# Optimization experiments

Hardware: AMD Instinct MI355X
Metric: run time of the kernel (lower is better)

## Reference

```python
import jax, jax.numpy as jnp
import numpy as np

B, S, D, H = 512, 256, 2, 256


def _lstm_cell(x, h, c, W_ih, W_hh, b_ih, b_hh):
    # PyTorch gate order: i, f, g, o
    gates = x @ W_ih.T + b_ih + h @ W_hh.T + b_hh
    i, f, g, o = jnp.split(gates, 4, axis=-1)
    c_new = jax.nn.sigmoid(f) * c + jax.nn.sigmoid(i) * jnp.tanh(g)
    h_new = jax.nn.sigmoid(o) * jnp.tanh(c_new)
    return h_new, c_new


def setup_inputs() -> dict:
    key = jax.random.key(0)
    ks = jax.random.split(key, 9)
    bound = 1.0 / np.sqrt(H)
    u = lambda k, shp: jax.random.uniform(k, shp, jnp.float32, -bound, bound)
    return {
        "inputs": jax.random.normal(ks[0], (B, S, D), jnp.float32),
        "enc_W_ih": u(ks[1], (4 * H, D)),
        "enc_W_hh": u(ks[2], (4 * H, H)),
        "enc_b_ih": u(ks[3], (4 * H,)),
        "enc_b_hh": u(ks[4], (4 * H,)),
        "dec_W_ih": u(ks[5], (4 * H, H)),
        "dec_W_hh": u(ks[6], (4 * H, H)),
        "dec_b_ih": u(ks[7], (4 * H,)),
        "dec_b_hh": u(ks[8], (4 * H,)),
    }


def reference(inputs, enc_W_ih, enc_W_hh, enc_b_ih, enc_b_hh,
              dec_W_ih, dec_W_hh, dec_b_ih, dec_b_hh):
    bsz, seq_len, _ = inputs.shape
    hid = enc_W_hh.shape[1]

    # ---- encoder LSTM (batch_first), h0 = c0 = 0 ----
    h0 = jnp.zeros((bsz, hid), inputs.dtype)
    c0 = jnp.zeros((bsz, hid), inputs.dtype)

    def enc_step(carry, x_t):
        h, c = carry
        h, c = _lstm_cell(x_t, h, c, enc_W_ih, enc_W_hh, enc_b_ih, enc_b_hh)
        return (h, c), h

    (h_last, c_last), enc_out_t = jax.lax.scan(enc_step, (h0, c0), inputs.transpose(1, 0, 2))
    enc_out = enc_out_t.transpose(1, 0, 2)  # [B, S, H]

    key = jax.random.key(42)
    keys = jax.random.split(key, seq_len)
    dec_in0 = jnp.zeros((bsz, hid), inputs.dtype)
    mask0 = jnp.zeros((bsz, seq_len), dtype=bool)
    rows = jnp.arange(bsz)

    def dec_step(carry, k):
        dec_in, h, c, mask = carry
        h, c = _lstm_cell(dec_in, h, c, dec_W_ih, dec_W_hh, dec_b_ih, dec_b_hh)
        scores = jnp.einsum('bsh,bh->bs', enc_out, h)          # bmm attention
        scores = jnp.where(mask, -jnp.inf, scores)             # mask visited
        idx = jax.random.categorical(k, scores, axis=1)        # multinomial(softmax)
        mask = mask.at[rows, idx].set(True)
        dec_in = jnp.take_along_axis(enc_out, idx[:, None, None], axis=1)[:, 0, :]
        return (dec_in, h, c, mask), idx

    _, indices_t = jax.lax.scan(dec_step, (dec_in0, h_last, c_last, mask0), keys)
    return indices_t.T  # [B, S] int
```

## Files before the change

### kernel.cpp

```cpp
#include <hip/hip_runtime.h>
#include <cstdint>
#include <cstddef>


typedef float v4f __attribute__((ext_vector_type(4)));
typedef float v2f __attribute__((ext_vector_type(2)));
typedef unsigned long long u64;

#define WS_HX_OFF     0x000000u
#define WS_GX_OFF     0x100000u
#define WS_AMX_OFF    0x200000u
#define WS_GFLAG_OFF  0x204000u
#define WS_SYNC_BYTES 0x205000u
#define WS_ENCW2_OFF  0x300000u
#define WS_DECWI4_OFF 0x400000u
#define WS_DECWH4_OFF 0x500000u
#define WS_ENCK4_OFF  0x600000u
#define WS_NEEDED     ((size_t)WS_ENCK4_OFF + (size_t)512 * 64 * 256 * 16)

__device__ __forceinline__ unsigned rotl32(unsigned x, int r) {
  return (x << r) | (x >> (32 - r));
}
__device__ __forceinline__ float sigm(float x) { return 1.f / (1.f + expf(-x)); }

__device__ __forceinline__ u64 pk(unsigned tag, unsigned payload) {
  return ((u64)tag << 32) | (u64)payload;
}
__device__ __forceinline__ unsigned spinrd(u64* p, unsigned tag) {
  u64 v = atomicAdd(p, 0ull);
  while ((unsigned)(v >> 32) != tag) {
    __builtin_amdgcn_s_sleep(2);
    v = atomicAdd(p, 0ull);
  }
  return (unsigned)v;
}

__device__ __forceinline__ void tf2(unsigned k0, unsigned k1,
                                    unsigned& x0, unsigned& x1) {
  const unsigned k2 = k0 ^ k1 ^ 0x1BD11BDAu;
  x0 += k0; x1 += k1;
  x0 += x1; x1 = rotl32(x1, 13); x1 ^= x0;
  x0 += x1; x1 = rotl32(x1, 15); x1 ^= x0;
  x0 += x1; x1 = rotl32(x1, 26); x1 ^= x0;
  x0 += x1; x1 = rotl32(x1,  6); x1 ^= x0;
  x0 += k1; x1 += k2 + 1u;
  x0 += x1; x1 = rotl32(x1, 17); x1 ^= x0;
  x0 += x1; x1 = rotl32(x1, 29); x1 ^= x0;
  x0 += x1; x1 = rotl32(x1, 16); x1 ^= x0;
  x0 += x1; x1 = rotl32(x1, 24); x1 ^= x0;
  x0 += k2; x1 += k0 + 2u;
  x0 += x1; x1 = rotl32(x1, 13); x1 ^= x0;
  x0 += x1; x1 = rotl32(x1, 15); x1 ^= x0;
  x0 += x1; x1 = rotl32(x1, 26); x1 ^= x0;
  x0 += x1; x1 = rotl32(x1,  6); x1 ^= x0;
  x0 += k0; x1 += k1 + 3u;
  x0 += x1; x1 = rotl32(x1, 17); x1 ^= x0;
  x0 += x1; x1 = rotl32(x1, 29); x1 ^= x0;
  x0 += x1; x1 = rotl32(x1, 16); x1 ^= x0;
  x0 += x1; x1 = rotl32(x1, 24); x1 ^= x0;
  x0 += k1; x1 += k2 + 4u;
  x0 += x1; x1 = rotl32(x1, 13); x1 ^= x0;
  x0 += x1; x1 = rotl32(x1, 15); x1 ^= x0;
  x0 += x1; x1 = rotl32(x1, 26); x1 ^= x0;
  x0 += x1; x1 = rotl32(x1,  6); x1 ^= x0;
  x0 += k2; x1 += k0 + 5u;
}

__global__ void repack_k(const float* __restrict__ eWh,
                         const float* __restrict__ dWi,
                         const float* __restrict__ dWh,
                         float* __restrict__ ws) {
  float* encW2 = (float*)((char*)ws + WS_ENCW2_OFF);
  float* decWi4 = (float*)((char*)ws + WS_DECWI4_OFF);
  float* decWh4 = (float*)((char*)ws + WS_DECWH4_OFF);
  const int n = blockIdx.x * blockDim.x + threadIdx.x;
  if (n >= 65536) return;
  const int k = n >> 8, u = n & 255;
#pragma unroll
  for (int g = 0; g < 4; ++g) {
    const int src = ((g << 8) + u) * 256 + k;
    decWi4[(n << 2) + g] = dWi[src];
    decWh4[(n << 2) + g] = dWh[src];
    encW2[(((g >> 1) << 16) + n) * 2 + (g & 1)] = eWh[src];
  }
}

__global__ void __launch_bounds__(1024)
ptrnet_kernel(const float* __restrict__ inp,
              const float* __restrict__ eWi,
              const float* __restrict__ eBi, const float* __restrict__ eBh,
              const float* __restrict__ dBi, const float* __restrict__ dBh,
              int* __restrict__ out,
              float* __restrict__ ws) {
  const int tid  = threadIdx.x;
  const int wave = tid >> 6, l = tid & 63;
  const int kq   = wave >> 2;
  const int uw   = wave & 3;
  const int uP   = (uw << 6) | l;
  const int k4b  = kq << 4;

  const int g    = blockIdx.x & 127;
  const int H    = blockIdx.x >> 7;
  const int b0   = g << 2;
  const int ubase = H << 7;
  const int pbase = ubase ^ 128;
  const int sbase = H << 7;

  const int isP2 = tid < 512;
  const int bD = tid >> 7;
  const int uL = tid & 127;
  const int uD = ubase | uL;
  const int bGD = b0 + bD;

  const v2f* encW2o = (const v2f*)((char*)ws + WS_ENCW2_OFF) + (H << 16);
  const v4f* decWi4 = (const v4f*)((char*)ws + WS_DECWI4_OFF);
  const v4f* decWh4 = (const v4f*)((char*)ws + WS_DECWH4_OFF);
  v4f* encK4 = (v4f*)((char*)ws + WS_ENCK4_OFF);

  u64* hxAll  = (u64*)((char*)ws + WS_HX_OFF);
  u64* hxMe   = hxAll + (size_t)g * 1024 + (size_t)H * 512;
  u64* hxYo   = hxAll + (size_t)g * 1024 + (size_t)(1 - H) * 512;
  u64* gxAll  = (u64*)((char*)ws + WS_GX_OFF);
  u64* gxMe   = gxAll + (size_t)g * 1024 + (size_t)H * 512;
  u64* gxYo   = gxAll + (size_t)g * 1024 + (size_t)(1 - H) * 512;
  u64* amxAll = (u64*)((char*)ws + WS_AMX_OFF);
  u64* amxMe  = amxAll + (size_t)g * 16 + (size_t)H * 8;
  u64* amxYo  = amxAll + (size_t)g * 16 + (size_t)(1 - H) * 8;
  u64* gfAll  = (u64*)((char*)ws + WS_GFLAG_OFF);
  u64* gflagMe = gfAll + (size_t)g * 2 + (size_t)H;
  u64* gflagYo = gfAll + (size_t)g * 2 + (size_t)(1 - H);

  __shared__ __align__(16) float hsF[2][1024];
  __shared__ __align__(16) v4f dinV[256];
  __shared__ __align__(16) v4f red[17][256];
  __shared__ unsigned char maskC[4][128];
  __shared__ float partV[4][2];
  __shared__ int   partI[4][2];
  __shared__ float oVs[4]; __shared__ int oIs[4];
  __shared__ float eVs[4]; __shared__ int eIs[4];
  v2f* red2 = (v2f*)&red[0][0];

  const int uB = isP2 ? uD : 0;
  const float ebi_ = eBi[uB] + eBh[uB];
  const float ebf_ = eBi[256 + uB] + eBh[256 + uB];
  const float ebg_ = eBi[512 + uB] + eBh[512 + uB];
  const float ebo_ = eBi[768 + uB] + eBh[768 + uB];
  const float wxi0 = eWi[2 * uB], wxi1 = eWi[2 * uB + 1];
  const float wxf0 = eWi[2 * (256 + uB)], wxf1 = eWi[2 * (256 + uB) + 1];
  const float wxg0 = eWi[2 * (512 + uB)], wxg1 = eWi[2 * (512 + uB) + 1];
  const float wxo0 = eWi[2 * (768 + uB)], wxo1 = eWi[2 * (768 + uB) + 1];

  hsF[0][tid] = 0.f;
  __syncthreads();

  float cD = 0.f;
  int p = 0;

  for (int t = 0; t < 256; ++t) {
    {
      v2f a0 = (v2f)0.f, a1 = (v2f)0.f, a2 = (v2f)0.f, a3 = (v2f)0.f;
      const v2f* Wp = encW2o + uP;
      const v4f* hq = (const v4f*)&hsF[p][0];
#pragma unroll 2
      for (int kk = 0; kk < 16; ++kk) {
        const int k4 = k4b + kk;
        const v2f w0 = Wp[(k4 * 4 + 0) << 8];
        const v2f w1 = Wp[(k4 * 4 + 1) << 8];
        const v2f w2 = Wp[(k4 * 4 + 2) << 8];
        const v2f w3 = Wp[(k4 * 4 + 3) << 8];
        const v4f h0 = hq[k4];
        const v4f h1 = hq[64 + k4];
        const v4f h2 = hq[128 + k4];
        const v4f h3 = hq[192 + k4];
        a0 += w0 * h0.x + w1 * h0.y + w2 * h0.z + w3 * h0.w;
        a1 += w0 * h1.x + w1 * h1.y + w2 * h1.z + w3 * h1.w;
        a2 += w0 * h2.x + w1 * h2.y + w2 * h2.z + w3 * h2.w;
        a3 += w0 * h3.x + w1 * h3.y + w2 * h3.z + w3 * h3.w;
      }
      red2[(((kq << 2) | 0) << 8) + uP] = a0;
      red2[(((kq << 2) | 1) << 8) + uP] = a1;
      red2[(((kq << 2) | 2) << 8) + uP] = a2;
      red2[(((kq << 2) | 3) << 8) + uP] = a3;
    }
    __syncthreads();

    if (isP2) {
      const int upub = pbase | uL;
      v2f gx = red2[(bD << 8) + upub];
      gx += red2[((4 + bD) << 8) + upub];
      gx += red2[((8 + bD) << 8) + upub];
      gx += red2[((12 + bD) << 8) + upub];
      const u64 pkd = ((u64)__float_as_uint(gx.y) << 32) | (u64)__float_as_uint(gx.x);
      atomicExch(&gxMe[(bD << 7) | uL], pkd);
    }
    __syncthreads();
    if (tid == 0) {
      atomicExch(gflagMe, pk(0xB0000001u + (unsigned)t, 0u));
      (void)spinrd(gflagYo, 0xB0000001u + (unsigned)t);
    }
    __syncthreads();

    if (isP2) {
      v2f own = red2[(bD << 8) + uD];
      own += red2[((4 + bD) << 8) + uD];
      own += red2[((8 + bD) << 8) + uD];
      own += red2[((12 + bD) << 8) + uD];
      const u64 pw = atomicAdd(&gxYo[(bD << 7) | uL], 0ull);
      const float ox = __uint_as_float((unsigned)pw);
      const float oy = __uint_as_float((unsigned)(pw >> 32));
      const float gvI = H ? ox : own.x;
      const float gvF = H ? oy : own.y;
      const float gvG = H ? own.x : ox;
      const float gvO = H ? own.y : oy;
      const float2 xv = *(const float2*)(inp + (((bGD) << 8) + t) * 2);
      const float ai = gvI + ebi_ + wxi0 * xv.x + wxi1 * xv.y;
      const float af = gvF + ebf_ + wxf0 * xv.x + wxf1 * xv.y;
      const float ag = gvG + ebg_ + wxg0 * xv.x + wxg1 * xv.y;
      const float ao = gvO + ebo_ + wxo0 * xv.x + wxo1 * xv.y;
      const float iv = sigm(ai), fv = sigm(af), gva = tanhf(ag), ov = sigm(ao);
      cD = fv * cD + iv * gva;
      const float hn = ov * tanhf(cD);
      hsF[p ^ 1][(bD << 8) | uD] = hn;
      ((float*)encK4)[(((bGD << 6) + (uD >> 2)) << 10) + (t << 2) + (uD & 3)] = hn;
      atomicExch(&hxMe[(bD << 7) | uL], pk(0xC0000001u + (unsigned)t, __float_as_uint(hn)));
      const unsigned pw2 = spinrd(&hxYo[(bD << 7) | uL], 0xC0000001u + (unsigned)t);
      hsF[p ^ 1][(bD << 8) | pbase | uL] = __uint_as_float(pw2);
    }
    __syncthreads();
    p ^= 1;
  }

  float dbi2 = 0.f, dbf2 = 0.f, dbg2 = 0.f, dbo2 = 0.f;
  if (isP2) {
    dbi2 = dBi[uD] + dBh[uD];
    dbf2 = dBi[256 + uD] + dBh[256 + uD];
    dbg2 = dBi[512 + uD] + dBh[512 + uD];
    dbo2 = dBi[768 + uD] + dBh[768 + uD];
  }
  const int aw  = wave - 8;
  const int bAt = aw >> 1;
  const int sL  = ((aw & 1) << 6) | l;
  const int sG  = sbase | sL;
  const int bGt = b0 + bAt;
  if (wave >= 8) maskC[bAt][sL] = 0;
  const int kqD  = wave >> 1;
  const int k4bD = kqD << 4;
  const int uPD  = ubase | ((wave & 1) << 6) | l;
  const float NEG_INF = __int_as_float((int)0xff800000);
  __syncthreads();

  {
    v4f a0 = (v4f)0.f, a1 = (v4f)0.f, a2 = (v4f)0.f, a3 = (v4f)0.f;
    const v4f* Wh = decWh4 + uP;
    const v4f* hq = (const v4f*)&hsF[p][0];
#pragma unroll 2
    for (int kk = 0; kk < 16; ++kk) {
      const int k4 = k4b + kk;
      const v4f w0 = Wh[(k4 * 4 + 0) << 8];
      const v4f w1 = Wh[(k4 * 4 + 1) << 8];
      const v4f w2 = Wh[(k4 * 4 + 2) << 8];
      const v4f w3 = Wh[(k4 * 4 + 3) << 8];
      const v4f h0 = hq[k4];
      const v4f h1 = hq[64 + k4];
      const v4f h2 = hq[128 + k4];
      const v4f h3 = hq[192 + k4];
      a0 += w0 * h0.x + w1 * h0.y + w2 * h0.z + w3 * h0.w;
      a1 += w0 * h1.x + w1 * h1.y + w2 * h1.z + w3 * h1.w;
      a2 += w0 * h2.x + w1 * h2.y + w2 * h2.z + w3 * h2.w;
      a3 += w0 * h3.x + w1 * h3.y + w2 * h3.z + w3 * h3.w;
    }
    red[(kq << 2) | 0][uP] = a0;
    red[(kq << 2) | 1][uP] = a1;
    red[(kq << 2) | 2][uP] = a2;
    red[(kq << 2) | 3][uP] = a3;
    __syncthreads();
    if (isP2) {
      const v4f gv = red[bD][uD] + red[4 + bD][uD] + red[8 + bD][uD] + red[12 + bD][uD];
      const float iv = sigm(gv.x + dbi2), fv = sigm(gv.y + dbf2);
      const float gva = tanhf(gv.z + dbg2), ov = sigm(gv.w + dbo2);
      cD = fv * cD + iv * gva;
      const float hn = ov * tanhf(cD);
      hsF[p ^ 1][(bD << 8) | uD] = hn;
      atomicExch(&hxMe[(bD << 7) | uL], pk(0xA5000000u, __float_as_uint(hn)));
      const unsigned pw = spinrd(&hxYo[(bD << 7) | uL], 0xA5000000u);
      hsF[p ^ 1][(bD << 8) | pbase | uL] = __uint_as_float(pw);
    }
    __syncthreads();
    p ^= 1;
  }

#define WINNER(B, WI) { float _wv = oVs[B]; int _wi = oIs[B];                 \
    const float _ev = eVs[B]; const int _ei = eIs[B];                         \
    if (_ev > _wv || (_ev == _wv && _ei < _wi)) { _wi = _ei; }                \
    WI = _wi; }

  for (int t = 0; t < 256; ++t) {
    const unsigned tagA = 0xA5000001u + 2u * (unsigned)t;
    const unsigned tagH = 0xA5000002u + 2u * (unsigned)t;
    const v4f* hq = (const v4f*)&hsF[p][0];

    if (wave < 8) {
      v4f a0 = (v4f)0.f, a1 = (v4f)0.f, a2 = (v4f)0.f, a3 = (v4f)0.f;
      const v4f* Wh = decWh4 + uPD;
#pragma unroll 2
      for (int kk = 0; kk < 16; ++kk) {
        const int k4 = k4bD + kk;
        const v4f w0 = Wh[(k4 * 4 + 0) << 8];
        const v4f w1 = Wh[(k4 * 4 + 1) << 8];
        const v4f w2 = Wh[(k4 * 4 + 2) << 8];
        const v4f w3 = Wh[(k4 * 4 + 3) << 8];
        const v4f h0 = hq[k4];
        const v4f h1 = hq[64 + k4];
        const v4f h2 = hq[128 + k4];
        const v4f h3 = hq[192 + k4];
        a0 += w0 * h0.x + w1 * h0.y + w2 * h0.z + w3 * h0.w;
        a1 += w0 * h1.x + w1 * h1.y + w2 * h1.z + w3 * h1.w;
        a2 += w0 * h2.x + w1 * h2.y + w2 * h2.z + w3 * h2.w;
        a3 += w0 * h3.x + w1 * h3.y + w2 * h3.z + w3 * h3.w;
      }
      red[(kqD << 2) | 0][uPD] = a0;
      red[(kqD << 2) | 1][uPD] = a1;
      red[(kqD << 2) | 2][uPD] = a2;
      red[(kqD << 2) | 3][uPD] = a3;
    } else {
      const int masked = maskC[bAt][sL];
      float sc = 0.f;
      if (!masked) {
        const v4f* E = encK4 + (bGt << 14) + sG;
        const v4f* hq2 = hq + (bAt << 6);
#pragma unroll 4
        for (int k4 = 0; k4 < 64; ++k4) {
          const v4f ev = E[k4 << 8];
          const v4f hv = hq2[k4];
          sc += ev.x * hv.x + ev.y * hv.y + ev.z * hv.z + ev.w * hv.w;
        }
      }
      unsigned bits;
      {
        unsigned kk0 = 0u, kk1 = (unsigned)t;
        tf2(0u, 42u, kk0, kk1);
        unsigned y0 = 0u, y1 = (unsigned)((bGt << 8) + sG);
        tf2(kk0, kk1, y0, y1);
        bits = y0 ^ y1;
      }
      const float fr = __uint_as_float((bits >> 9) | 0x3f800000u) - 1.0f;
      const float uu = (fr > 0.f) ? fr : 1.17549435e-38f;
      const float gum = -logf(-logf(uu));
      float bv = masked ? NEG_INF : (sc + gum);
      int bi = sG;
#pragma unroll
      for (int off = 32; off; off >>= 1) {
        const float ov2 = __shfl_xor(bv, off, 64);
        const int oi2 = __shfl_xor(bi, off, 64);
        if (ov2 > bv || (ov2 == bv && oi2 < bi)) { bv = ov2; bi = oi2; }
      }
      if (l == 0) { partV[bAt][aw & 1] = bv; partI[bAt][aw & 1] = bi; }
    }
    __syncthreads();

    if (tid < 4) {
      float v0 = partV[tid][0]; int i0 = partI[tid][0];
      const float v1 = partV[tid][1];
      if (v1 > v0) { v0 = v1; i0 = partI[tid][1]; }
      oVs[tid] = v0; oIs[tid] = i0;
      atomicExch(&amxMe[tid * 2 + 0], pk(tagA, __float_as_uint(v0)));
      atomicExch(&amxMe[tid * 2 + 1], pk(tagA, (unsigned)i0));
    }
    if (tid >= 64 && tid < 72) {
      const int j = tid - 64;
      const unsigned pw = spinrd(&amxYo[j], tagA);
      if (j & 1) eIs[j >> 1] = (int)pw;
      else       eVs[j >> 1] = __uint_as_float(pw);
    }
    __syncthreads();

    if (wave >= 8) {
      int wi; WINNER(bAt, wi);
      if (sG == wi) maskC[bAt][sL] = 1;
    }
    if (H == 0 && tid < 4) {
      int wi; WINNER(tid, wi);
      out[((b0 + tid) << 8) + t] = wi;
    }
    if (tid < 256) {
      const int bb = tid >> 6, k4s = tid & 63;
      int wi; WINNER(bb, wi);
      dinV[tid] = encK4[((((b0 + bb) << 6) | k4s) << 8) + wi];
    }
    __syncthreads();

    if (t == 255) break;

    if (wave < 8) {
      v4f a0 = red[(kqD << 2) | 0][uPD];
      v4f a1 = red[(kqD << 2) | 1][uPD];
      v4f a2 = red[(kqD << 2) | 2][uPD];
      v4f a3 = red[(kqD << 2) | 3][uPD];
      const v4f* Wi = decWi4 + uPD;
#pragma unroll 2
      for (int kk = 0; kk < 16; ++kk) {
        const int k4 = k4bD + kk;
        const v4f w0 = Wi[(k4 * 4 + 0) << 8];
        const v4f w1 = Wi[(k4 * 4 + 1) << 8];
        const v4f w2 = Wi[(k4 * 4 + 2) << 8];
        const v4f w3 = Wi[(k4 * 4 + 3) << 8];
        const v4f d0 = dinV[k4];
        const v4f d1 = dinV[64 + k4];
        const v4f d2 = dinV[128 + k4];
        const v4f d3 = dinV[192 + k4];
        a0 += w0 * d0.x + w1 * d0.y + w2 * d0.z + w3 * d0.w;
        a1 += w0 * d1.x + w1 * d1.y + w2 * d1.z + w3 * d1.w;
        a2 += w0 * d2.x + w1 * d2.y + w2 * d2.z + w3 * d2.w;
        a3 += w0 * d3.x + w1 * d3.y + w2 * d3.z + w3 * d3.w;
      }
      red[(kqD << 2) | 0][uPD] = a0;
      red[(kqD << 2) | 1][uPD] = a1;
      red[(kqD << 2) | 2][uPD] = a2;
      red[(kqD << 2) | 3][uPD] = a3;
    }
    __syncthreads();

    if (isP2) {
      const v4f gv = red[bD][uD] + red[4 + bD][uD] + red[8 + bD][uD] + red[12 + bD][uD];
      const float iv = sigm(gv.x + dbi2), fv = sigm(gv.y + dbf2);
      const float gva = tanhf(gv.z + dbg2), ov = sigm(gv.w + dbo2);
      cD = fv * cD + iv * gva;
      const float hn = ov * tanhf(cD);
      hsF[p ^ 1][(bD << 8) | uD] = hn;
      atomicExch(&hxMe[(bD << 7) | uL], pk(tagH, __float_as_uint(hn)));
      const unsigned pw = spinrd(&hxYo[(bD << 7) | uL], tagH);
      hsF[p ^ 1][(bD << 8) | pbase | uL] = __uint_as_float(pw);
    }
    __syncthreads();
    p ^= 1;
  }
#undef WINNER
}

extern "C" void kernel_launch(void* const* d_in, const int* in_sizes, int n_in,
                              void* d_out, int out_size, void* d_ws, size_t ws_size,
                              hipStream_t stream) {
  (void)in_sizes; (void)n_in; (void)out_size;
  if (ws_size < WS_NEEDED) return;

  const float* inp = (const float*)d_in[0];
  const float* eWi = (const float*)d_in[1];
  const float* eWh = (const float*)d_in[2];
  const float* eBi = (const float*)d_in[3];
  const float* eBh = (const float*)d_in[4];
  const float* dWi = (const float*)d_in[5];
  const float* dWh = (const float*)d_in[6];
  const float* dBi = (const float*)d_in[7];
  const float* dBh = (const float*)d_in[8];
  int* out = (int*)d_out;
  float* wsf = (float*)d_ws;

  hipMemsetAsync((char*)d_ws, 0, WS_SYNC_BYTES, stream);
  hipLaunchKernelGGL(repack_k, dim3(256), dim3(256), 0, stream, eWh, dWi, dWh, wsf);
  hipLaunchKernelGGL(ptrnet_kernel, dim3(256), dim3(1024), 0, stream,
                     inp, eWi, eBi, eBh, dBi, dBh, out, wsf);
}
```

Baseline: 9.350 ms.

## Replace flag barrier with per-element tagged gate exchange between paired blocks

```diff
diff --git a/kernel.cpp b/kernel.cpp
--- a/kernel.cpp
+++ b/kernel.cpp
@@ -9,9 +9,7 @@
 
 #define WS_HX_OFF     0x000000u
 #define WS_GX_OFF     0x100000u
-#define WS_AMX_OFF    0x200000u
-#define WS_GFLAG_OFF  0x204000u
-#define WS_SYNC_BYTES 0x205000u
+#define WS_SYNC_BYTES 0x300000u
 #define WS_ENCW2_OFF  0x300000u
 #define WS_DECWI4_OFF 0x400000u
 #define WS_DECWH4_OFF 0x500000u
@@ -121,14 +119,10 @@
   u64* hxMe   = hxAll + (size_t)g * 1024 + (size_t)H * 512;
   u64* hxYo   = hxAll + (size_t)g * 1024 + (size_t)(1 - H) * 512;
   u64* gxAll  = (u64*)((char*)ws + WS_GX_OFF);
-  u64* gxMe   = gxAll + (size_t)g * 1024 + (size_t)H * 512;
-  u64* gxYo   = gxAll + (size_t)g * 1024 + (size_t)(1 - H) * 512;
-  u64* amxAll = (u64*)((char*)ws + WS_AMX_OFF);
-  u64* amxMe  = amxAll + (size_t)g * 16 + (size_t)H * 8;
-  u64* amxYo  = amxAll + (size_t)g * 16 + (size_t)(1 - H) * 8;
-  u64* gfAll  = (u64*)((char*)ws + WS_GFLAG_OFF);
-  u64* gflagMe = gfAll + (size_t)g * 2 + (size_t)H;
-  u64* gflagYo = gfAll + (size_t)g * 2 + (size_t)(1 - H);
+  u64* gxMe   = gxAll + ((size_t)g * 2 + (size_t)H) * 1024;
+  u64* gxYo   = gxAll + ((size_t)g * 2 + (size_t)(1 - H)) * 1024;
+  u64* amxMe  = gxMe;
+  u64* amxYo  = gxYo;
 
   __shared__ __align__(16) float hsF[2][1024];
   __shared__ __align__(16) v4f dinV[256];
@@ -184,30 +178,25 @@
     }
     __syncthreads();
 
-    if (isP2) {
-      const int upub = pbase | uL;
-      v2f gx = red2[(bD << 8) + upub];
-      gx += red2[((4 + bD) << 8) + upub];
-      gx += red2[((8 + bD) << 8) + upub];
-      gx += red2[((12 + bD) << 8) + upub];
-      const u64 pkd = ((u64)__float_as_uint(gx.y) << 32) | (u64)__float_as_uint(gx.x);
-      atomicExch(&gxMe[(bD << 7) | uL], pkd);
-    }
-    __syncthreads();
-    if (tid == 0) {
-      atomicExch(gflagMe, pk(0xB0000001u + (unsigned)t, 0u));
-      (void)spinrd(gflagYo, 0xB0000001u + (unsigned)t);
-    }
-    __syncthreads();
-
-    if (isP2) {
+    const unsigned tagG = 0xD0000000u + (unsigned)t;
+    if (!isP2) {
+      const int ix = tid - 512;
+      const int bP = ix >> 7, uLp = ix & 127;
+      const int upub = pbase | uLp;
+      v2f gx = red2[(bP << 8) + upub];
+      gx += red2[((4 + bP) << 8) + upub];
+      gx += red2[((8 + bP) << 8) + upub];
+      gx += red2[((12 + bP) << 8) + upub];
+      atomicExch(&gxMe[(ix << 1) + 0], pk(tagG, __float_as_uint(gx.x)));
+      atomicExch(&gxMe[(ix << 1) + 1], pk(tagG, __float_as_uint(gx.y)));
+    } else {
       v2f own = red2[(bD << 8) + uD];
       own += red2[((4 + bD) << 8) + uD];
       own += red2[((8 + bD) << 8) + uD];
       own += red2[((12 + bD) << 8) + uD];
-      const u64 pw = atomicAdd(&gxYo[(bD << 7) | uL], 0ull);
-      const float ox = __uint_as_float((unsigned)pw);
-      const float oy = __uint_as_float((unsigned)(pw >> 32));
+      const int ix = tid;
+      const float ox = __uint_as_float(spinrd(&gxYo[(ix << 1) + 0], tagG));
+      const float oy = __uint_as_float(spinrd(&gxYo[(ix << 1) + 1], tagG));
       const float gvI = H ? ox : own.x;
       const float gvF = H ? oy : own.y;
       const float gvG = H ? own.x : ox;
```

New measurement: 9.817 ms. 5.0% more time.
